# Kernel optimization log

Hardware: AMD Instinct MI355X
Metric: run time of the kernel (lower is better)

Reference implementation:

```python
import jax, jax.numpy as jnp
import numpy as np

N_NODES = 100000
IN_DIM = 500
HID = 64
N_CLASSES = 47
N_EDGES = 1200000
K_LAYERS = 2


def _spmm_rownorm(edge_index, h, n):
    # Row-normalized D^{-1} A @ h via gather + segment_sum over edge list.
    src, dst = edge_index[0], edge_index[1]
    ones = jnp.ones(src.shape[0], dtype=h.dtype)
    deg = jax.ops.segment_sum(ones, src, num_segments=n)
    inv_deg = 1.0 / jnp.maximum(deg, 1.0)
    msg = h[dst] * inv_deg[src][:, None]  # [E, HID]
    return jax.ops.segment_sum(msg, src, num_segments=n)  # [N, HID]


def setup_inputs() -> dict:
    key = jax.random.key(0)
    ks = jax.random.split(key, 12)
    x = jax.random.normal(ks[0], (N_NODES, IN_DIM), dtype=jnp.float32)
    edge_index_1 = jax.random.randint(ks[1], (2, N_EDGES), 0, N_NODES, dtype=jnp.int32)
    edge_index_2 = jax.random.randint(ks[2], (2, N_EDGES), 0, N_NODES, dtype=jnp.int32)
    s = 0.02
    W_embed = jax.random.normal(ks[3], (IN_DIM, HID), dtype=jnp.float32) * s
    b_embed = jnp.zeros((HID,), dtype=jnp.float32)
    W0 = jax.random.normal(ks[4], (4 * HID, HID), dtype=jnp.float32) * s
    b0 = jnp.zeros((HID,), dtype=jnp.float32)
    W1 = jax.random.normal(ks[5], (4 * HID, HID), dtype=jnp.float32) * s
    b1 = jnp.zeros((HID,), dtype=jnp.float32)
    Wc = jax.random.normal(ks[6], (HID * (K_LAYERS + 1), N_CLASSES), dtype=jnp.float32) * s
    bc = jnp.zeros((N_CLASSES,), dtype=jnp.float32)
    return {"x": x, "edge_index_1": edge_index_1, "edge_index_2": edge_index_2,
            "W_embed": W_embed, "b_embed": b_embed, "W0": W0, "b0": b0,
            "W1": W1, "b1": b1, "Wc": Wc, "bc": bc}


def reference(x, edge_index_1, edge_index_2, W_embed, b_embed, W0, b0, W1, b1, Wc, bc):
    n = x.shape[0]
    r0 = jax.nn.relu(x @ W_embed + b_embed)  # dropout = identity in eval
    reps = [r0]
    r_prev = r0
    for (W, b) in ((W0, b0), (W1, b1)):
        n1 = _spmm_rownorm(edge_index_1, r_prev, n)
        n2 = _spmm_rownorm(edge_index_2, r_prev, n)
        concat = jnp.concatenate([r_prev, n1, r_prev, n2], axis=1)  # ego separation
        r_k = jax.nn.relu(concat @ W + b)
        reps.append(r_k)
        r_prev = r_k
    emb = jnp.concatenate(reps, axis=1)  # [N, HID*(K+1)]
    logits = emb @ Wc + bc
    return logits
```

## Files before the change

kernel.cpp:

```cpp
#include <hip/hip_runtime.h>

namespace {

constexpr int N  = 100000;
constexpr int KD = 500;
constexpr int E  = 1200000;
constexpr int NC = 47;

constexpr int M2  = 2 * N;
constexpr int E2  = 2 * E;
constexpr int NB  = 391;
constexpr int AB  = 586;
constexpr int EBMAX = 8192;

typedef __attribute__((ext_vector_type(8))) short short8;
typedef __attribute__((ext_vector_type(4))) float f32x4;

__device__ __forceinline__ ushort f2bf(float f) {
    union { float f; uint u; } c; c.f = f;
    uint u = c.u + 0x7fffu + ((c.u >> 16) & 1);
    return (ushort)(u >> 16);
}
__device__ __forceinline__ float bflo(uint v) { union { uint u; float f; } c; c.u = v << 16;        return c.f; }
__device__ __forceinline__ float bfhi(uint v) { union { uint u; float f; } c; c.u = v & 0xffff0000u; return c.f; }


__global__ __launch_bounds__(256) void prep_all(const float* __restrict__ We, const float* __restrict__ W0,
                                                const float* __restrict__ W1, const float* __restrict__ Wc,
                                                const float* __restrict__ bc,
                                                int* __restrict__ bucketCnt, ushort* __restrict__ wtE,
                                                ushort* __restrict__ wf0, ushort* __restrict__ wf1,
                                                ushort* __restrict__ wct, float* __restrict__ bcp) {
    int i = blockIdx.x * 256 + threadIdx.x;
    if (i < NB + 1) bucketCnt[i] = 0;
    if (i < 64 * 512) {
        int c = i >> 9, k = i & 511;
        wtE[i] = f2bf(k < KD ? We[k * 64 + c] : 0.f);
    }
    if (i < 64 * 192) {
        int c = i / 192, k = i % 192;
        float v0, v1;
        if (k < 64)       { v0 = W0[k * 64 + c] + W0[(128 + k) * 64 + c];
                            v1 = W1[k * 64 + c] + W1[(128 + k) * 64 + c]; }
        else if (k < 128) { v0 = W0[k * 64 + c]; v1 = W1[k * 64 + c]; }
        else              { v0 = W0[(k + 64) * 64 + c]; v1 = W1[(k + 64) * 64 + c]; }
        wf0[i] = f2bf(v0);
        wf1[i] = f2bf(v1);
        wct[i] = f2bf(c < NC ? Wc[k * NC + c] : 0.f);
    }
    if (i < 64) bcp[i] = (i < NC) ? bc[i] : 0.f;
}


__global__ __launch_bounds__(256) void bucket_count(const int* __restrict__ src1, const int* __restrict__ src2,
                                                    int* __restrict__ bucketCnt) {
    __shared__ int h[NB];
    int t = threadIdx.x;
    for (int b = t; b < NB; b += 256) h[b] = 0;
    __syncthreads();
    #pragma unroll
    for (int q = 0; q < 16; ++q) {
        int i = blockIdx.x * 4096 + q * 256 + t;
        if (i < E2) {
            int g = i >= E;
            int idx = i - g * E;
            int s = g ? src2[idx] : src1[idx];
            atomicAdd(&h[(g * N + s) >> 9], 1);
        }
    }
    __syncthreads();
    for (int b = t; b < NB; b += 256)
        if (h[b]) atomicAdd(&bucketCnt[b], h[b]);
}

__global__ __launch_bounds__(256) void bucket_scan(const int* __restrict__ bucketCnt,
                                                   int* __restrict__ base, int* __restrict__ cursor) {
    __shared__ int h[512];
    __shared__ int ps[256];
    __shared__ int ex[512];
    int t = threadIdx.x;
    h[t] = (t < NB) ? bucketCnt[t] : 0;
    h[t + 256] = (t + 256 < NB) ? bucketCnt[t + 256] : 0;
    __syncthreads();
    int pv = h[2 * t] + h[2 * t + 1];
    ps[t] = pv;
    __syncthreads();
    for (int off = 1; off < 256; off <<= 1) {
        int x = (t >= off) ? ps[t - off] : 0;
        __syncthreads();
        ps[t] += x;
        __syncthreads();
    }
    int e2 = ps[t] - pv;
    ex[2 * t] = e2;
    ex[2 * t + 1] = e2 + h[2 * t];
    __syncthreads();
    for (int k = t; k < NB; k += 256) {
        base[k]   = ex[k];
        cursor[k] = ex[k];
    }
    if (t == 0) base[NB] = E2;
}

__global__ __launch_bounds__(256) void bucket_scatter(const int* __restrict__ src1, const int* __restrict__ dst1,
                                                      const int* __restrict__ src2, const int* __restrict__ dst2,
                                                      int* __restrict__ cursor, uint* __restrict__ ebuf) {
    __shared__ int h[NB];
    __shared__ int claim[NB];
    int t = threadIdx.x;
    int mb[16];
    uint mu[16];
    for (int b = t; b < NB; b += 256) h[b] = 0;
    __syncthreads();
    #pragma unroll
    for (int q = 0; q < 16; ++q) {
        int i = blockIdx.x * 4096 + q * 256 + t;
        if (i < E2) {
            int g = i >= E;
            int idx = i - g * E;
            int s = g ? src2[idx] : src1[idx];
            int d = g ? dst2[idx] : dst1[idx];
            int v = g * N + s;
            mb[q] = v >> 9;
            mu[q] = ((uint)(v & 511) << 17) | (uint)d;
            atomicAdd(&h[mb[q]], 1);
        } else {
            mb[q] = -1;
            mu[q] = 0;
        }
    }
    __syncthreads();
    for (int b = t; b < NB; b += 256)
        claim[b] = h[b] ? atomicAdd(&cursor[b], h[b]) : 0;
    __syncthreads();
    for (int b = t; b < NB; b += 256) h[b] = 0;
    __syncthreads();
    #pragma unroll
    for (int q = 0; q < 16; ++q) {
        if (mb[q] >= 0) {
            int r = atomicAdd(&h[mb[q]], 1);
            ebuf[claim[mb[q]] + r] = mu[q];
        }
    }
}

__global__ __launch_bounds__(256) void csr_finalize(const uint* __restrict__ ebuf, const int* __restrict__ base,
                                                    int* __restrict__ rp, float* __restrict__ invd,
                                                    int* __restrict__ col) {
    __shared__ uint eb[EBMAX];
    __shared__ int h[512];
    __shared__ int ex[512];
    __shared__ int ps[256];
    int bid = blockIdx.x;
    int t = threadIdx.x;
    int b0 = base[bid];
    int cnt = base[bid + 1] - b0;
    if (cnt > EBMAX) cnt = EBMAX;
    h[t] = 0; h[t + 256] = 0;
    for (int j = t; j < cnt; j += 256) eb[j] = ebuf[b0 + j];
    __syncthreads();
    for (int j = t; j < cnt; j += 256) atomicAdd(&h[eb[j] >> 17], 1);
    __syncthreads();
    int pv = h[2 * t] + h[2 * t + 1];
    ps[t] = pv;
    __syncthreads();
    for (int off = 1; off < 256; off <<= 1) {
        int x = (t >= off) ? ps[t - off] : 0;
        __syncthreads();
        ps[t] += x;
        __syncthreads();
    }
    int e2 = ps[t] - pv;
    ex[2 * t] = e2;
    ex[2 * t + 1] = e2 + h[2 * t];
    __syncthreads();
    #pragma unroll
    for (int q = 0; q < 2; ++q) {
        int k = q * 256 + t;
        int n = bid * 512 + k;
        if (n < M2) {
            rp[n] = b0 + ex[k];
            int dv = h[k];
            invd[n] = 1.0f / (float)(dv > 1 ? dv : 1);
        }
    }
    if (bid == 0 && t == 0) rp[M2] = E2;
    __syncthreads();
    for (int j = t; j < cnt; j += 256) {
        uint u = eb[j];
        int ls = u >> 17;
        int r = atomicAdd(&ex[ls], 1);
        col[b0 + r] = (int)(u & 0x1FFFFu) * 384;
    }
}


__device__ __forceinline__ void stageB(const ushort* __restrict__ Wt, int ldw, int k0, short* Bs) {
    const int tid = threadIdx.x;
    #pragma unroll
    for (int i = 0; i < 2; ++i) {
        int idx = tid + i * 256;
        int c = idx >> 3, qc = (idx & 7) * 8;
        uint4 v = *reinterpret_cast<const uint4*>(Wt + (size_t)c * ldw + k0 + qc);
        *reinterpret_cast<uint4*>(Bs + (((c << 6) + qc) ^ ((c & 7) << 3))) = v;
    }
}

__device__ __forceinline__ void mma64(const short* As, const short* Bs, f32x4 acc[2][4]) {
    const int lane = threadIdx.x & 63;
    const int wrow = (threadIdx.x >> 6) * 32;
    const int llo = lane & 15, lhi = lane >> 4;
    #pragma unroll
    for (int kf = 0; kf < 2; ++kf) {
        const int kb = kf * 32 + lhi * 8;
        short8 a[2], b[4];
        #pragma unroll
        for (int m = 0; m < 2; ++m) {
            int r = wrow + m * 16 + llo;
            a[m] = *reinterpret_cast<const short8*>(As + (((r << 6) + kb) ^ ((r & 7) << 3)));
        }
        #pragma unroll
        for (int n = 0; n < 4; ++n) {
            int c = n * 16 + llo;
            b[n] = *reinterpret_cast<const short8*>(Bs + (((c << 6) + kb) ^ ((c & 7) << 3)));
        }
        #pragma unroll
        for (int m = 0; m < 2; ++m)
            #pragma unroll
            for (int n = 0; n < 4; ++n)
                acc[m][n] = __builtin_amdgcn_mfma_f32_16x16x32_bf16(a[m], b[n], acc[m][n], 0, 0, 0);
    }
}

template<bool OUTF32>
__device__ __forceinline__ void epilogue(f32x4 acc[2][4], const float* __restrict__ bias,
                                         void* out, int ldo, int ocols, int relu, int rbase) {
    const int lane = threadIdx.x & 63;
    const int wrow = (threadIdx.x >> 6) * 32;
    #pragma unroll
    for (int m = 0; m < 2; ++m) {
        #pragma unroll
        for (int r = 0; r < 4; ++r) {
            int orow = rbase + wrow + m * 16 + (lane >> 4) * 4 + r;
            if (orow >= N) continue;
            #pragma unroll
            for (int n = 0; n < 4; ++n) {
                int c = n * 16 + (lane & 15);
                float v = acc[m][n][r] + bias[c];
                if (relu) v = fmaxf(v, 0.f);
                if (OUTF32) {
                    if (c < ocols) ((float*)out)[(size_t)orow * ldo + c] = v;
                } else {
                    ((ushort*)out)[(size_t)orow * ldo + c] = f2bf(v);
                }
            }
        }
    }
}

__global__ __launch_bounds__(256) void gemm_embed(const float* __restrict__ x,
                                                  const ushort* __restrict__ WtE,
                                                  const float* __restrict__ bias,
                                                  ushort* __restrict__ out) {
    __shared__ short As[128 * 64];
    __shared__ short Bs[64 * 64];
    const int tid = threadIdx.x;
    const int rbase = blockIdx.x * 128;
    f32x4 acc[2][4] = {};
    for (int k0 = 0; k0 < 512; k0 += 64) {
        __syncthreads();
        #pragma unroll
        for (int i = 0; i < 8; ++i) {
            int idx = tid + i * 256;
            int r = idx >> 4, qc = (idx & 15) * 4;
            int grow = rbase + r;
            float4 v = {0.f, 0.f, 0.f, 0.f};
            if (grow < N && k0 + qc < KD) v = *reinterpret_cast<const float4*>(x + (size_t)grow * KD + k0 + qc);
            uint2 p;
            p.x = (uint)f2bf(v.x) | ((uint)f2bf(v.y) << 16);
            p.y = (uint)f2bf(v.z) | ((uint)f2bf(v.w) << 16);
            *reinterpret_cast<uint2*>(As + (((r << 6) + qc) ^ ((r & 7) << 3))) = p;
        }
        stageB(WtE, 512, k0, Bs);
        __syncthreads();
        mma64(As, Bs, acc);
    }
    epilogue<false>(acc, bias, out, 192, 64, 1, rbase);
}

template<bool OUTF32>
__global__ __launch_bounds__(256) void gemm3(const ushort* __restrict__ a0, int lda0,
                                             const ushort* __restrict__ a1, int lda1,
                                             const ushort* __restrict__ a2, int lda2,
                                             const ushort* __restrict__ Wt,
                                             const float* __restrict__ bias,
                                             void* out, int ldo, int ocols, int relu) {
    __shared__ short As[128 * 64];
    __shared__ short Bs[64 * 64];
    const int tid = threadIdx.x;
    const int rbase = blockIdx.x * 128;
    f32x4 acc[2][4] = {};
    const ushort* aseg[3] = {a0, a1, a2};
    const int ldas[3] = {lda0, lda1, lda2};
    #pragma unroll
    for (int seg = 0; seg < 3; ++seg) {
        const ushort* A = aseg[seg];
        const int lda = ldas[seg];
        __syncthreads();
        #pragma unroll
        for (int i = 0; i < 4; ++i) {
            int idx = tid + i * 256;
            int r = idx >> 3, qc = (idx & 7) * 8;
            int grow = rbase + r;
            uint4 v = {0u, 0u, 0u, 0u};
            if (grow < N) v = *reinterpret_cast<const uint4*>(A + (size_t)grow * lda + qc);
            *reinterpret_cast<uint4*>(As + (((r << 6) + qc) ^ ((r & 7) << 3))) = v;
        }
        stageB(Wt, 192, seg * 64, Bs);
        __syncthreads();
        mma64(As, Bs, acc);
    }
    epilogue<OUTF32>(acc, bias, out, ldo, ocols, relu, rbase);
}


__global__ __launch_bounds__(256) void spmm7(const int* __restrict__ rp, const int* __restrict__ col,
                                             const float* __restrict__ invd,
                                             const ushort* __restrict__ table, int colOff,
                                             ushort* __restrict__ n1b, ushort* __restrict__ n2b) {
    int gid = (blockIdx.x * 256 + threadIdx.x) >> 3;
    int ls = threadIdx.x & 7;
    if (gid >= M2) return;
    const char* hb = (const char*)(table + colOff) + ls * 16;
    float w = invd[gid];
    int s = rp[gid], e = rp[gid + 1];
    float a0=0.f,a1=0.f,a2=0.f,a3=0.f,a4=0.f,a5=0.f,a6=0.f,a7=0.f;
    for (int j = s; j < e; j += 4) {
        int e1 = e - 1;
        int i1 = j + 1 < e ? j + 1 : e1;
        int i2 = j + 2 < e ? j + 2 : e1;
        int i3 = j + 3 < e ? j + 3 : e1;
        int o0 = col[j], o1 = col[i1], o2 = col[i2], o3 = col[i3];
        uint4 v0 = *reinterpret_cast<const uint4*>(hb + o0);
        uint4 v1 = *reinterpret_cast<const uint4*>(hb + o1);
        uint4 v2 = *reinterpret_cast<const uint4*>(hb + o2);
        uint4 v3 = *reinterpret_cast<const uint4*>(hb + o3);
        float w1 = j + 1 < e ? 1.f : 0.f;
        float w2 = j + 2 < e ? 1.f : 0.f;
        float w3 = j + 3 < e ? 1.f : 0.f;
        a0 += bflo(v0.x); a1 += bfhi(v0.x); a2 += bflo(v0.y); a3 += bfhi(v0.y);
        a4 += bflo(v0.z); a5 += bfhi(v0.z); a6 += bflo(v0.w); a7 += bfhi(v0.w);
        a0 = fmaf(w1, bflo(v1.x), a0); a1 = fmaf(w1, bfhi(v1.x), a1);
        a2 = fmaf(w1, bflo(v1.y), a2); a3 = fmaf(w1, bfhi(v1.y), a3);
        a4 = fmaf(w1, bflo(v1.z), a4); a5 = fmaf(w1, bfhi(v1.z), a5);
        a6 = fmaf(w1, bflo(v1.w), a6); a7 = fmaf(w1, bfhi(v1.w), a7);
        a0 = fmaf(w2, bflo(v2.x), a0); a1 = fmaf(w2, bfhi(v2.x), a1);
        a2 = fmaf(w2, bflo(v2.y), a2); a3 = fmaf(w2, bfhi(v2.y), a3);
        a4 = fmaf(w2, bflo(v2.z), a4); a5 = fmaf(w2, bfhi(v2.z), a5);
        a6 = fmaf(w2, bflo(v2.w), a6); a7 = fmaf(w2, bfhi(v2.w), a7);
        a0 = fmaf(w3, bflo(v3.x), a0); a1 = fmaf(w3, bfhi(v3.x), a1);
        a2 = fmaf(w3, bflo(v3.y), a2); a3 = fmaf(w3, bfhi(v3.y), a3);
        a4 = fmaf(w3, bflo(v3.z), a4); a5 = fmaf(w3, bfhi(v3.z), a5);
        a6 = fmaf(w3, bflo(v3.w), a6); a7 = fmaf(w3, bfhi(v3.w), a7);
    }
    int g = gid >= N;
    int node = gid - g * N;
    ushort* op = g ? n2b : n1b;
    uint4 o;
    o.x = (uint)f2bf(a0 * w) | ((uint)f2bf(a1 * w) << 16);
    o.y = (uint)f2bf(a2 * w) | ((uint)f2bf(a3 * w) << 16);
    o.z = (uint)f2bf(a4 * w) | ((uint)f2bf(a5 * w) << 16);
    o.w = (uint)f2bf(a6 * w) | ((uint)f2bf(a7 * w) << 16);
    *reinterpret_cast<uint4*>(op + (size_t)node * 64 + ls * 8) = o;
}

}

extern "C" void kernel_launch(void* const* d_in, const int* in_sizes, int n_in,
                              void* d_out, int out_size, void* d_ws, size_t ws_size,
                              hipStream_t stream) {
    const float* x       = (const float*)d_in[0];
    const int*   ei1     = (const int*)d_in[1];
    const int*   ei2     = (const int*)d_in[2];
    const float* W_embed = (const float*)d_in[3];
    const float* b_embed = (const float*)d_in[4];
    const float* W0      = (const float*)d_in[5];
    const float* b0      = (const float*)d_in[6];
    const float* W1      = (const float*)d_in[7];
    const float* b1      = (const float*)d_in[8];
    const float* Wc      = (const float*)d_in[9];
    const float* bc      = (const float*)d_in[10];
    float* out = (float*)d_out;

    char* ws = (char*)d_ws;
    size_t off = 0;
    auto alloc = [&](size_t bytes) -> void* {
        void* p = ws + off;
        off += (bytes + 255) & ~(size_t)255;
        return p;
    };

    ushort* embB  = (ushort*)alloc((size_t)N * 192 * 2);
    ushort* n1b   = (ushort*)alloc((size_t)N * 64 * 2);
    ushort* n2b   = (ushort*)alloc((size_t)N * 64 * 2);
    int*    col   = (int*)alloc((size_t)E2 * 4);
    uint*   ebuf  = (uint*)alloc((size_t)E2 * 4);
    int*    rp    = (int*)alloc((size_t)(M2 + 1) * 4);
    float*  invd  = (float*)alloc((size_t)M2 * 4);
    int*    bcnt  = (int*)alloc((NB + 1) * 4);
    int*    bbase = (int*)alloc((NB + 1) * 4);
    int*    bcur  = (int*)alloc((NB + 1) * 4);
    ushort* wtE   = (ushort*)alloc(64 * 512 * 2);
    ushort* weff0 = (ushort*)alloc(64 * 192 * 2);
    ushort* weff1 = (ushort*)alloc(64 * 192 * 2);
    ushort* wct   = (ushort*)alloc(64 * 192 * 2);
    float*  bcp   = (float*)alloc(64 * 4);
    if (off > ws_size) return;

    const int* src1 = ei1, *dst1 = ei1 + E;
    const int* src2 = ei2, *dst2 = ei2 + E;

    const int GB = (N + 127) / 128;
    const int PB = (M2 * 8 + 255) / 256;

    prep_all<<<128, 256, 0, stream>>>(W_embed, W0, W1, Wc, bc, bcnt, wtE, weff0, weff1, wct, bcp);

    bucket_count<<<AB, 256, 0, stream>>>(src1, src2, bcnt);
    bucket_scan<<<1, 256, 0, stream>>>(bcnt, bbase, bcur);
    bucket_scatter<<<AB, 256, 0, stream>>>(src1, dst1, src2, dst2, bcur, ebuf);
    csr_finalize<<<NB, 256, 0, stream>>>(ebuf, bbase, rp, invd, col);

    gemm_embed<<<GB, 256, 0, stream>>>(x, wtE, b_embed, embB);

    for (int layer = 0; layer < 2; ++layer) {
        const ushort* rprev = embB + 64 * layer;
        spmm7<<<PB, 256, 0, stream>>>(rp, col, invd, embB, 64 * layer, n1b, n2b);
        const ushort* Wl = (layer == 0) ? weff0 : weff1;
        const float*  bl = (layer == 0) ? b0 : b1;
        gemm3<false><<<GB, 256, 0, stream>>>(rprev, 192, n1b, 64, n2b, 64, Wl, bl,
                                             embB + 64 * (layer + 1), 192, 64, 1);
    }

    gemm3<true><<<GB, 256, 0, stream>>>(embB, 192, embB + 64, 192, embB + 128, 192, wct, bcp,
                                        out, NC, NC, 0);
}
```

Measured before the change: 250.7 us.

## Split SpMM gather into column slabs and drop bucket count/scan passes

Stores the hidden features also in four column-sliced slabs (16 bf16 per node), so each SpMM pass gathers 32-byte rows from a smaller table that fits cache better. SpMM is launched four times per layer, once per slab, with two lanes per row. The GEMM reads neighbour aggregates from the slab layout. Separately, CSR construction gives each bucket a fixed-capacity region of EBMAX entries, which removes the count and scan kernels at the cost of more workspace. The risk is that a bucket holding more than EBMAX edges loses edges silently, and the extra slab writes and launches add overhead.

```diff
diff --git a/kernel.cpp b/kernel.cpp
--- a/kernel.cpp
+++ b/kernel.cpp
@@ -12,6 +12,7 @@
 constexpr int NB  = 391;
 constexpr int AB  = 586;
 constexpr int EBMAX = 8192;
+constexpr int SB  = (M2 * 2 + 255) / 256;
 
 typedef __attribute__((ext_vector_type(8))) short short8;
 typedef __attribute__((ext_vector_type(4))) float f32x4;
@@ -28,11 +29,11 @@
 __global__ __launch_bounds__(256) void prep_all(const float* __restrict__ We, const float* __restrict__ W0,
                                                 const float* __restrict__ W1, const float* __restrict__ Wc,
                                                 const float* __restrict__ bc,
-                                                int* __restrict__ bucketCnt, ushort* __restrict__ wtE,
+                                                int* __restrict__ cursor, ushort* __restrict__ wtE,
                                                 ushort* __restrict__ wf0, ushort* __restrict__ wf1,
                                                 ushort* __restrict__ wct, float* __restrict__ bcp) {
     int i = blockIdx.x * 256 + threadIdx.x;
-    if (i < NB + 1) bucketCnt[i] = 0;
+    if (i < NB) cursor[i] = i * EBMAX;
     if (i < 64 * 512) {
         int c = i >> 9, k = i & 511;
         wtE[i] = f2bf(k < KD ? We[k * 64 + c] : 0.f);
@@ -51,56 +52,6 @@
     if (i < 64) bcp[i] = (i < NC) ? bc[i] : 0.f;
 }
 
-
-__global__ __launch_bounds__(256) void bucket_count(const int* __restrict__ src1, const int* __restrict__ src2,
-                                                    int* __restrict__ bucketCnt) {
-    __shared__ int h[NB];
-    int t = threadIdx.x;
-    for (int b = t; b < NB; b += 256) h[b] = 0;
-    __syncthreads();
-    #pragma unroll
-    for (int q = 0; q < 16; ++q) {
-        int i = blockIdx.x * 4096 + q * 256 + t;
-        if (i < E2) {
-            int g = i >= E;
-            int idx = i - g * E;
-            int s = g ? src2[idx] : src1[idx];
-            atomicAdd(&h[(g * N + s) >> 9], 1);
-        }
-    }
-    __syncthreads();
-    for (int b = t; b < NB; b += 256)
-        if (h[b]) atomicAdd(&bucketCnt[b], h[b]);
-}
-
-__global__ __launch_bounds__(256) void bucket_scan(const int* __restrict__ bucketCnt,
-                                                   int* __restrict__ base, int* __restrict__ cursor) {
-    __shared__ int h[512];
-    __shared__ int ps[256];
-    __shared__ int ex[512];
-    int t = threadIdx.x;
-    h[t] = (t < NB) ? bucketCnt[t] : 0;
-    h[t + 256] = (t + 256 < NB) ? bucketCnt[t + 256] : 0;
-    __syncthreads();
-    int pv = h[2 * t] + h[2 * t + 1];
-    ps[t] = pv;
-    __syncthreads();
-    for (int off = 1; off < 256; off <<= 1) {
-        int x = (t >= off) ? ps[t - off] : 0;
-        __syncthreads();
-        ps[t] += x;
-        __syncthreads();
-    }
-    int e2 = ps[t] - pv;
-    ex[2 * t] = e2;
-    ex[2 * t + 1] = e2 + h[2 * t];
-    __syncthreads();
-    for (int k = t; k < NB; k += 256) {
-        base[k]   = ex[k];
-        cursor[k] = ex[k];
-    }
-    if (t == 0) base[NB] = E2;
-}
 
 __global__ __launch_bounds__(256) void bucket_scatter(const int* __restrict__ src1, const int* __restrict__ dst1,
                                                       const int* __restrict__ src2, const int* __restrict__ dst2,
@@ -144,18 +95,19 @@
     }
 }
 
-__global__ __launch_bounds__(256) void csr_finalize(const uint* __restrict__ ebuf, const int* __restrict__ base,
-                                                    int* __restrict__ rp, float* __restrict__ invd,
-                                                    int* __restrict__ col) {
+__global__ __launch_bounds__(256) void csr_finalize(const uint* __restrict__ ebuf, const int* __restrict__ cursor,
+                                                    int* __restrict__ rp, int* __restrict__ rpe,
+                                                    float* __restrict__ invd, int* __restrict__ col) {
     __shared__ uint eb[EBMAX];
     __shared__ int h[512];
     __shared__ int ex[512];
     __shared__ int ps[256];
     int bid = blockIdx.x;
     int t = threadIdx.x;
-    int b0 = base[bid];
-    int cnt = base[bid + 1] - b0;
+    int b0 = bid * EBMAX;
+    int cnt = cursor[bid] - b0;
     if (cnt > EBMAX) cnt = EBMAX;
+    if (cnt < 0) cnt = 0;
     h[t] = 0; h[t + 256] = 0;
     for (int j = t; j < cnt; j += 256) eb[j] = ebuf[b0 + j];
     __syncthreads();
@@ -179,18 +131,19 @@
         int k = q * 256 + t;
         int n = bid * 512 + k;
         if (n < M2) {
-            rp[n] = b0 + ex[k];
+            int st = b0 + ex[k];
             int dv = h[k];
+            rp[n]  = st;
+            rpe[n] = st + dv;
             invd[n] = 1.0f / (float)(dv > 1 ? dv : 1);
         }
     }
-    if (bid == 0 && t == 0) rp[M2] = E2;
     __syncthreads();
     for (int j = t; j < cnt; j += 256) {
         uint u = eb[j];
         int ls = u >> 17;
         int r = atomicAdd(&ex[ls], 1);
-        col[b0 + r] = (int)(u & 0x1FFFFu) * 384;
+        col[b0 + r] = (int)(u & 0x1FFFFu) * 32;
     }
 }
 
@@ -234,7 +187,8 @@
 
 template<bool OUTF32>
 __device__ __forceinline__ void epilogue(f32x4 acc[2][4], const float* __restrict__ bias,
-                                         void* out, int ldo, int ocols, int relu, int rbase) {
+                                         void* out, int ldo, int ocols, int relu, int rbase,
+                                         ushort* __restrict__ slab) {
     const int lane = threadIdx.x & 63;
     const int wrow = (threadIdx.x >> 6) * 32;
     #pragma unroll
@@ -251,7 +205,9 @@
                 if (OUTF32) {
                     if (c < ocols) ((float*)out)[(size_t)orow * ldo + c] = v;
                 } else {
-                    ((ushort*)out)[(size_t)orow * ldo + c] = f2bf(v);
+                    ushort bv = f2bf(v);
+                    ((ushort*)out)[(size_t)orow * ldo + c] = bv;
+                    if (slab) slab[(size_t)(c >> 4) * (N * 16) + (size_t)orow * 16 + (c & 15)] = bv;
                 }
             }
         }
@@ -261,7 +217,8 @@
 __global__ __launch_bounds__(256) void gemm_embed(const float* __restrict__ x,
                                                   const ushort* __restrict__ WtE,
                                                   const float* __restrict__ bias,
-                                                  ushort* __restrict__ out) {
+                                                  ushort* __restrict__ out,
+                                                  ushort* __restrict__ slab) {
     __shared__ short As[128 * 64];
     __shared__ short Bs[64 * 64];
     const int tid = threadIdx.x;
@@ -285,16 +242,17 @@
         __syncthreads();
         mma64(As, Bs, acc);
     }
-    epilogue<false>(acc, bias, out, 192, 64, 1, rbase);
-}
-
-template<bool OUTF32>
+    epilogue<false>(acc, bias, out, 192, 64, 1, rbase, slab);
+}
+
+template<bool OUTF32, bool SLABIN>
 __global__ __launch_bounds__(256) void gemm3(const ushort* __restrict__ a0, int lda0,
                                              const ushort* __restrict__ a1, int lda1,
                                              const ushort* __restrict__ a2, int lda2,
                                              const ushort* __restrict__ Wt,
                                              const float* __restrict__ bias,
-                                             void* out, int ldo, int ocols, int relu) {
+                                             void* out, int ldo, int ocols, int relu,
+                                             ushort* __restrict__ slabOut) {
     __shared__ short As[128 * 64];
     __shared__ short Bs[64 * 64];
     const int tid = threadIdx.x;
@@ -313,38 +271,44 @@
             int r = idx >> 3, qc = (idx & 7) * 8;
             int grow = rbase + r;
             uint4 v = {0u, 0u, 0u, 0u};
-            if (grow < N) v = *reinterpret_cast<const uint4*>(A + (size_t)grow * lda + qc);
+            if (grow < N) {
+                if (SLABIN && seg > 0)
+                    v = *reinterpret_cast<const uint4*>(A + (size_t)(qc >> 4) * (N * 16)
+                                                          + (size_t)grow * 16 + (qc & 15));
+                else
+                    v = *reinterpret_cast<const uint4*>(A + (size_t)grow * lda + qc);
+            }
             *reinterpret_cast<uint4*>(As + (((r << 6) + qc) ^ ((r & 7) << 3))) = v;
         }
         stageB(Wt, 192, seg * 64, Bs);
         __syncthreads();
         mma64(As, Bs, acc);
     }
-    epilogue<OUTF32>(acc, bias, out, ldo, ocols, relu, rbase);
-}
-
-
-__global__ __launch_bounds__(256) void spmm7(const int* __restrict__ rp, const int* __restrict__ col,
-                                             const float* __restrict__ invd,
-                                             const ushort* __restrict__ table, int colOff,
-                                             ushort* __restrict__ n1b, ushort* __restrict__ n2b) {
-    int gid = (blockIdx.x * 256 + threadIdx.x) >> 3;
-    int ls = threadIdx.x & 7;
+    epilogue<OUTF32>(acc, bias, out, ldo, ocols, relu, rbase, slabOut);
+}
+
+
+__global__ __launch_bounds__(256) void spmm_slice(const int* __restrict__ rp, const int* __restrict__ rpe,
+                                                  const int* __restrict__ col, const float* __restrict__ invd,
+                                                  const ushort* __restrict__ gslab,
+                                                  ushort* __restrict__ o1, ushort* __restrict__ o2) {
+    int gid = (blockIdx.x * 256 + threadIdx.x) >> 1;
+    int ls = threadIdx.x & 1;
     if (gid >= M2) return;
-    const char* hb = (const char*)(table + colOff) + ls * 16;
+    const char* hb = (const char*)gslab + ls * 16;
     float w = invd[gid];
-    int s = rp[gid], e = rp[gid + 1];
+    int s = rp[gid], e = rpe[gid];
     float a0=0.f,a1=0.f,a2=0.f,a3=0.f,a4=0.f,a5=0.f,a6=0.f,a7=0.f;
     for (int j = s; j < e; j += 4) {
         int e1 = e - 1;
         int i1 = j + 1 < e ? j + 1 : e1;
         int i2 = j + 2 < e ? j + 2 : e1;
         int i3 = j + 3 < e ? j + 3 : e1;
-        int o0 = col[j], o1 = col[i1], o2 = col[i2], o3 = col[i3];
+        int o0 = col[j], o1c = col[i1], o2c = col[i2], o3c = col[i3];
         uint4 v0 = *reinterpret_cast<const uint4*>(hb + o0);
-        uint4 v1 = *reinterpret_cast<const uint4*>(hb + o1);
-        uint4 v2 = *reinterpret_cast<const uint4*>(hb + o2);
-        uint4 v3 = *reinterpret_cast<const uint4*>(hb + o3);
+        uint4 v1 = *reinterpret_cast<const uint4*>(hb + o1c);
+        uint4 v2 = *reinterpret_cast<const uint4*>(hb + o2c);
+        uint4 v3 = *reinterpret_cast<const uint4*>(hb + o3c);
         float w1 = j + 1 < e ? 1.f : 0.f;
         float w2 = j + 2 < e ? 1.f : 0.f;
         float w3 = j + 3 < e ? 1.f : 0.f;
@@ -365,13 +329,13 @@
     }
     int g = gid >= N;
     int node = gid - g * N;
-    ushort* op = g ? n2b : n1b;
+    ushort* op = g ? o2 : o1;
     uint4 o;
     o.x = (uint)f2bf(a0 * w) | ((uint)f2bf(a1 * w) << 16);
     o.y = (uint)f2bf(a2 * w) | ((uint)f2bf(a3 * w) << 16);
     o.z = (uint)f2bf(a4 * w) | ((uint)f2bf(a5 * w) << 16);
     o.w = (uint)f2bf(a6 * w) | ((uint)f2bf(a7 * w) << 16);
-    *reinterpret_cast<uint4*>(op + (size_t)node * 64 + ls * 8) = o;
+    *reinterpret_cast<uint4*>((char*)op + (size_t)node * 32 + ls * 16) = o;
 }
 
 }
@@ -401,14 +365,14 @@
     };
 
     ushort* embB  = (ushort*)alloc((size_t)N * 192 * 2);
-    ushort* n1b   = (ushort*)alloc((size_t)N * 64 * 2);
-    ushort* n2b   = (ushort*)alloc((size_t)N * 64 * 2);
-    int*    col   = (int*)alloc((size_t)E2 * 4);
-    uint*   ebuf  = (uint*)alloc((size_t)E2 * 4);
-    int*    rp    = (int*)alloc((size_t)(M2 + 1) * 4);
+    ushort* gslab = (ushort*)alloc((size_t)4 * N * 16 * 2);
+    ushort* o1s   = (ushort*)alloc((size_t)4 * N * 16 * 2);
+    ushort* o2s   = (ushort*)alloc((size_t)4 * N * 16 * 2);
+    int*    col   = (int*)alloc((size_t)NB * EBMAX * 4);
+    uint*   ebuf  = (uint*)alloc((size_t)NB * EBMAX * 4);
+    int*    rp    = (int*)alloc((size_t)M2 * 4);
+    int*    rpe   = (int*)alloc((size_t)M2 * 4);
     float*  invd  = (float*)alloc((size_t)M2 * 4);
-    int*    bcnt  = (int*)alloc((NB + 1) * 4);
-    int*    bbase = (int*)alloc((NB + 1) * 4);
     int*    bcur  = (int*)alloc((NB + 1) * 4);
     ushort* wtE   = (ushort*)alloc(64 * 512 * 2);
     ushort* weff0 = (ushort*)alloc(64 * 192 * 2);
@@ -421,26 +385,27 @@
     const int* src2 = ei2, *dst2 = ei2 + E;
 
     const int GB = (N + 127) / 128;
-    const int PB = (M2 * 8 + 255) / 256;
-
-    prep_all<<<128, 256, 0, stream>>>(W_embed, W0, W1, Wc, bc, bcnt, wtE, weff0, weff1, wct, bcp);
-
-    bucket_count<<<AB, 256, 0, stream>>>(src1, src2, bcnt);
-    bucket_scan<<<1, 256, 0, stream>>>(bcnt, bbase, bcur);
+
+    prep_all<<<128, 256, 0, stream>>>(W_embed, W0, W1, Wc, bc, bcur, wtE, weff0, weff1, wct, bcp);
+
     bucket_scatter<<<AB, 256, 0, stream>>>(src1, dst1, src2, dst2, bcur, ebuf);
-    csr_finalize<<<NB, 256, 0, stream>>>(ebuf, bbase, rp, invd, col);
-
-    gemm_embed<<<GB, 256, 0, stream>>>(x, wtE, b_embed, embB);
+    csr_finalize<<<NB, 256, 0, stream>>>(ebuf, bcur, rp, rpe, invd, col);
+
+    gemm_embed<<<GB, 256, 0, stream>>>(x, wtE, b_embed, embB, gslab);
 
     for (int layer = 0; layer < 2; ++layer) {
+        for (int s = 0; s < 4; ++s) {
+            size_t so = (size_t)s * N * 16;
+            spmm_slice<<<SB, 256, 0, stream>>>(rp, rpe, col, invd, gslab + so, o1s + so, o2s + so);
+        }
         const ushort* rprev = embB + 64 * layer;
-        spmm7<<<PB, 256, 0, stream>>>(rp, col, invd, embB, 64 * layer, n1b, n2b);
         const ushort* Wl = (layer == 0) ? weff0 : weff1;
         const float*  bl = (layer == 0) ? b0 : b1;
-        gemm3<false><<<GB, 256, 0, stream>>>(rprev, 192, n1b, 64, n2b, 64, Wl, bl,
-                                             embB + 64 * (layer + 1), 192, 64, 1);
-    }
-
-    gemm3<true><<<GB, 256, 0, stream>>>(embB, 192, embB + 64, 192, embB + 128, 192, wct, bcp,
-                                        out, NC, NC, 0);
-}
+        gemm3<false, true><<<GB, 256, 0, stream>>>(rprev, 192, o1s, 0, o2s, 0, Wl, bl,
+                                                   embB + 64 * (layer + 1), 192, 64, 1,
+                                                   (layer == 0) ? gslab : (ushort*)nullptr);
+    }
+
+    gemm3<true, false><<<GB, 256, 0, stream>>>(embB, 192, embB + 64, 192, embB + 128, 192, wct, bcp,
+                                               out, NC, NC, 0, nullptr);
+}
```

Measured after the change: 327.1 us. 1.3x slower.
